# Optimization experiments

Hardware: AMD Instinct MI355X
Metric: run time of the kernel (lower is better)

The kernel has to match this reference:

```python
import jax, jax.numpy as jnp
import numpy as np

B, C, F_IN, F_OUT = 2048, 63, 250, 250
NEG_SLOPE = 0.2
N = B * C  # flattened node count


def _build_edge_index():
    # fixed fully-connected (no self) graph over the FIRST 63 nodes only
    src = np.array([i for i in range(C) for j in range(C) if i != j], dtype=np.int32)
    dst = np.array([j for i in range(C) for j in range(C) if i != j], dtype=np.int32)
    # PyG GATConv add_self_loops=True: self loop for every node (num_nodes = N)
    loops = np.arange(N, dtype=np.int32)
    src = np.concatenate([src, loops])
    dst = np.concatenate([dst, loops])
    return jnp.asarray(np.stack([src, dst]))  # [2, E]


def setup_inputs() -> dict:
    key = jax.random.key(0)
    kx, kw, ks, kd = jax.random.split(key, 4)
    x = jax.random.normal(kx, (B, 1, C, F_IN), dtype=jnp.float32)
    # GATConv params (heads=1): lin weight, att_src, att_dst, bias
    W = jax.random.normal(kw, (F_IN, F_OUT), dtype=jnp.float32) / np.sqrt(F_IN)
    att_src = jax.random.normal(ks, (F_OUT,), dtype=jnp.float32) / np.sqrt(F_OUT)
    att_dst = jax.random.normal(kd, (F_OUT,), dtype=jnp.float32) / np.sqrt(F_OUT)
    bias = jnp.zeros((F_OUT,), dtype=jnp.float32)
    return {"x": x, "W": W, "att_src": att_src, "att_dst": att_dst,
            "bias": bias, "edge_index": _build_edge_index()}


def reference(x, W, att_src, att_dst, bias, edge_index):
    b, _, c, f = x.shape
    n = b * c
    h = x.reshape(n, f) @ W                      # [N, F_OUT]
    a_src = h @ att_src                          # [N]
    a_dst = h @ att_dst                          # [N]
    src, dst = edge_index[0], edge_index[1]
    e = jax.nn.leaky_relu(a_src[src] + a_dst[dst], NEG_SLOPE)  # [E]
    # segment softmax over incoming edges of each dst node (stable)
    m = jax.ops.segment_max(e, dst, num_segments=n)
    ex = jnp.exp(e - m[dst])
    denom = jax.ops.segment_sum(ex, dst, num_segments=n)
    alpha = ex / denom[dst]                      # [E]
    out = jax.ops.segment_sum(alpha[:, None] * h[src], dst, num_segments=n)
    out = out + bias
    return out.reshape(b, 1, c, -1)              # [B,1,63,F_OUT]
```

## Files before the change

### kernel.cpp

```cpp
#include <hip/hip_runtime.h>
#include <cstdint>
#include <cstddef>

#define M_TOTAL 129024
#define KDIM    250
#define NDIM    250
#define KPAD    256
#define BM      128
#define BN      128
#define BK      64
#define LSTR    72

typedef float  f32x4  __attribute__((ext_vector_type(4)));
typedef __bf16 bf16x8 __attribute__((ext_vector_type(8)));

static __device__ __forceinline__ unsigned short f2bf(float f) {
  unsigned u = __float_as_uint(f);
  u += 0x7fffu + ((u >> 16) & 1u);
  return (unsigned short)(u >> 16);
}

static __device__ __forceinline__ float wsum(float v) {
#pragma unroll
  for (int o = 32; o > 0; o >>= 1) v += __shfl_xor(v, o, 64);
  return v;
}
static __device__ __forceinline__ float wmaxr(float v) {
#pragma unroll
  for (int o = 32; o > 0; o >>= 1) v = fmaxf(v, __shfl_xor(v, o, 64));
  return v;
}

__global__ void wcvt_kernel(const float* __restrict__ W, unsigned short* __restrict__ WT) {
  int k = threadIdx.x;
  int n = blockIdx.x;
  unsigned short v = 0;
  if (k < KDIM) v = f2bf(W[(size_t)k * NDIM + n]);
  WT[(size_t)n * KPAD + k] = v;
}

__global__ __launch_bounds__(256) void gemm_kernel(
    const float* __restrict__ X, const unsigned short* __restrict__ WT,
    const float* __restrict__ bias, float* __restrict__ out,
    float* __restrict__ h63) {
  __shared__ unsigned short lA[BM * LSTR];
  __shared__ unsigned short lB[BN * LSTR];

  const int g      = blockIdx.x;
  const int xcd    = g & 7;
  const int j      = g >> 3;
  const int m_tile = (j >> 1) * 8 + xcd;
  const int n_tile = j & 1;
  const int mBase  = m_tile * BM;
  const int nBase  = n_tile * BN;

  const int tid  = threadIdx.x;
  const int lane = tid & 63;
  const int wid  = tid >> 6;
  const int wm   = wid >> 1;
  const int wn   = wid & 1;
  const int r16  = lane & 15;
  const int quad = lane >> 4;

  f32x4 acc[4][4];
#pragma unroll
  for (int mt = 0; mt < 4; ++mt)
#pragma unroll
    for (int nt = 0; nt < 4; ++nt)
      acc[mt][nt] = f32x4{0.f, 0.f, 0.f, 0.f};

  const int aq  = tid & 15;
  const int ar0 = tid >> 4;
  const int bc  = tid & 7;
  const int br0 = tid >> 3;

  for (int kt = 0; kt < KPAD / BK; ++kt) {
    const int k0 = kt * BK;
    {
      const int gk = k0 + aq * 4;
      const bool full = (gk + 3 < KDIM);
#pragma unroll
      for (int jj = 0; jj < 8; ++jj) {
        const int row = ar0 + jj * 16;
        const float* src = X + (size_t)(mBase + row) * KDIM + gk;
        float a0, a1, a2, a3;
        if (full) {
          float2 p0 = *reinterpret_cast<const float2*>(src);
          float2 p1 = *reinterpret_cast<const float2*>(src + 2);
          a0 = p0.x; a1 = p0.y; a2 = p1.x; a3 = p1.y;
        } else {
          a0 = (gk + 0 < KDIM) ? src[0] : 0.f;
          a1 = (gk + 1 < KDIM) ? src[1] : 0.f;
          a2 = (gk + 2 < KDIM) ? src[2] : 0.f;
          a3 = (gk + 3 < KDIM) ? src[3] : 0.f;
        }
        unsigned lo = (unsigned)f2bf(a0) | ((unsigned)f2bf(a1) << 16);
        unsigned hi = (unsigned)f2bf(a2) | ((unsigned)f2bf(a3) << 16);
        *reinterpret_cast<uint2*>(&lA[row * LSTR + aq * 4]) = make_uint2(lo, hi);
      }
    }
    {
#pragma unroll
      for (int jj = 0; jj < 4; ++jj) {
        const int row = br0 + jj * 32;
        const int n = nBase + row;
        uint4 v;
        if (n < NDIM) v = *reinterpret_cast<const uint4*>(WT + (size_t)n * KPAD + k0 + bc * 8);
        else          v = make_uint4(0u, 0u, 0u, 0u);
        *reinterpret_cast<uint4*>(&lB[row * LSTR + bc * 8]) = v;
      }
    }
    __syncthreads();
#pragma unroll
    for (int ks = 0; ks < 2; ++ks) {
      const int koff = ks * 32 + quad * 8;
      bf16x8 aF[4], bF[4];
#pragma unroll
      for (int mt = 0; mt < 4; ++mt)
        aF[mt] = *reinterpret_cast<const bf16x8*>(&lA[(wm * 64 + mt * 16 + r16) * LSTR + koff]);
#pragma unroll
      for (int nt = 0; nt < 4; ++nt)
        bF[nt] = *reinterpret_cast<const bf16x8*>(&lB[(wn * 64 + nt * 16 + r16) * LSTR + koff]);
#pragma unroll
      for (int mt = 0; mt < 4; ++mt)
#pragma unroll
        for (int nt = 0; nt < 4; ++nt)
          acc[mt][nt] = __builtin_amdgcn_mfma_f32_16x16x32_bf16(aF[mt], bF[nt], acc[mt][nt], 0, 0, 0);
    }
    __syncthreads();
  }

#pragma unroll
  for (int mt = 0; mt < 4; ++mt) {
#pragma unroll
    for (int nt = 0; nt < 4; ++nt) {
      const int col = nBase + wn * 64 + nt * 16 + r16;
      if (col < NDIM) {
        const float bv = bias[col];
        const int rbase = mBase + wm * 64 + mt * 16 + quad * 4;
        f32x4 a = acc[mt][nt];
#pragma unroll
        for (int i = 0; i < 4; ++i) {
          const int r = rbase + i;
          out[(size_t)r * NDIM + col] = a[i] + bv;
          if (r < 63) h63[r * NDIM + col] = a[i];
        }
      }
    }
  }
}

__global__ void att_kernel(const float* __restrict__ h, const float* __restrict__ att_src,
                           const float* __restrict__ att_dst, const float* __restrict__ bias,
                           float* __restrict__ out) {
  const int d = blockIdx.x;
  const int tid = threadIdx.x;
  const int lane = tid & 63;
  const int wid = tid >> 6;

  __shared__ float s_asrc[64];
  __shared__ float s_adst;
  __shared__ float s_alpha[64];

  for (int s = wid; s < 63; s += 4) {
    float sum = 0.f;
    for (int f = lane; f < NDIM; f += 64) sum += h[s * NDIM + f] * att_src[f];
    sum = wsum(sum);
    if (lane == 0) s_asrc[s] = sum;
  }
  if (wid == 0) {
    float sum = 0.f;
    for (int f = lane; f < NDIM; f += 64) sum += h[d * NDIM + f] * att_dst[f];
    sum = wsum(sum);
    if (lane == 0) s_adst = sum;
  }
  __syncthreads();

  if (wid == 0) {
    float e = -__builtin_inff();
    if (lane < 63) {
      float x = s_asrc[lane] + s_adst;
      e = (x > 0.f) ? x : 0.2f * x;
    }
    const float m = wmaxr(e);
    const float p = (lane < 63) ? expf(e - m) : 0.f;
    const float den = wsum(p);
    s_alpha[lane] = p / den;
  }
  __syncthreads();

  const int f = tid;
  if (f < NDIM) {
    float o = bias[f];
    for (int s = 0; s < 63; ++s) o += s_alpha[s] * h[s * NDIM + f];
    out[(size_t)d * NDIM + f] = o;
  }
}

extern "C" void kernel_launch(void* const* d_in, const int* in_sizes, int n_in,
                              void* d_out, int out_size, void* d_ws, size_t ws_size,
                              hipStream_t stream) {
  const float* X       = (const float*)d_in[0];
  const float* W       = (const float*)d_in[1];
  const float* att_src = (const float*)d_in[2];
  const float* att_dst = (const float*)d_in[3];
  const float* bias    = (const float*)d_in[4];
  float* out = (float*)d_out;

  unsigned short* WT = (unsigned short*)d_ws;
  float* h63 = (float*)((char*)d_ws + 131072);

  wcvt_kernel<<<NDIM, KPAD, 0, stream>>>(W, WT);
  gemm_kernel<<<(M_TOTAL / BM) * 2, 256, 0, stream>>>(X, WT, bias, out, h63);
  att_kernel<<<63, 256, 0, stream>>>(h63, att_src, att_dst, bias, out);
}
```

Before: 327.4 us.

## Restructure GEMM: full-N per block, register-resident pre-swizzled W fragments

The weight conversion kernel now writes W in MFMA fragment order, so each wave loads its B fragments straight into registers (4 n-tiles × 8 k-steps). Each block now covers a 64-row M tile across the full 256-column N, which removes the duplicate reads of X from two n-tile blocks. The whole A tile is loaded at once through coalesced float2 loads, converted to bf16 and stored in LDS with a single barrier, so the K loop no longer needs LDS round trips for B. The cost is high register pressure from 32 B fragments plus 32 float2 values under launch_bounds(256,2), and less latency hiding with only one load phase.

```diff
diff --git a/kernel.cpp b/kernel.cpp
--- a/kernel.cpp
+++ b/kernel.cpp
@@ -5,11 +5,8 @@
 #define M_TOTAL 129024
 #define KDIM    250
 #define NDIM    250
-#define KPAD    256
-#define BM      128
-#define BN      128
-#define BK      64
-#define LSTR    72
+#define BM      64
+#define LASTR   264
 
 typedef float  f32x4  __attribute__((ext_vector_type(4)));
 typedef __bf16 bf16x8 __attribute__((ext_vector_type(8)));
@@ -31,37 +28,72 @@
   return v;
 }
 
-__global__ void wcvt_kernel(const float* __restrict__ W, unsigned short* __restrict__ WT) {
-  int k = threadIdx.x;
-  int n = blockIdx.x;
-  unsigned short v = 0;
-  if (k < KDIM) v = f2bf(W[(size_t)k * NDIM + n]);
-  WT[(size_t)n * KPAD + k] = v;
-}
-
-__global__ __launch_bounds__(256) void gemm_kernel(
-    const float* __restrict__ X, const unsigned short* __restrict__ WT,
+__global__ void wcvt_kernel(const float* __restrict__ W, unsigned short* __restrict__ WTf) {
+  const int f     = blockIdx.x * 256 + threadIdx.x;
+  const int lane  = f & 63;
+  const int kk    = (f >> 6) & 7;
+  const int ntile = f >> 9;
+  const int n     = ntile * 16 + (lane & 15);
+  const int k0    = kk * 32 + (lane >> 4) * 8;
+  unsigned u[4];
+#pragma unroll
+  for (int p = 0; p < 4; ++p) {
+    const int ka = k0 + 2 * p, kb = k0 + 2 * p + 1;
+    unsigned short a = (n < NDIM && ka < KDIM) ? f2bf(W[(size_t)ka * NDIM + n]) : 0;
+    unsigned short b = (n < NDIM && kb < KDIM) ? f2bf(W[(size_t)kb * NDIM + n]) : 0;
+    u[p] = (unsigned)a | ((unsigned)b << 16);
+  }
+  *reinterpret_cast<uint4*>(WTf + (size_t)f * 8) = make_uint4(u[0], u[1], u[2], u[3]);
+}
+
+__global__ __launch_bounds__(256, 2) void gemm_kernel(
+    const float* __restrict__ X, const unsigned short* __restrict__ WTf,
     const float* __restrict__ bias, float* __restrict__ out,
     float* __restrict__ h63) {
-  __shared__ unsigned short lA[BM * LSTR];
-  __shared__ unsigned short lB[BN * LSTR];
-
-  const int g      = blockIdx.x;
-  const int xcd    = g & 7;
-  const int j      = g >> 3;
-  const int m_tile = (j >> 1) * 8 + xcd;
-  const int n_tile = j & 1;
-  const int mBase  = m_tile * BM;
-  const int nBase  = n_tile * BN;
-
+  __shared__ unsigned short lA[BM * LASTR];
+
+  const int mBase = blockIdx.x * BM;
   const int tid  = threadIdx.x;
   const int lane = tid & 63;
-  const int wid  = tid >> 6;
-  const int wm   = wid >> 1;
-  const int wn   = wid & 1;
+  const int w    = tid >> 6;
   const int r16  = lane & 15;
   const int quad = lane >> 4;
 
+  const float* Xs = X + (size_t)mBase * KDIM;
+
+  float2 av[32];
+#pragma unroll
+  for (int j = 0; j < 32; ++j) {
+    const int idx = j * 256 + tid;
+    if (j < 31 || tid < 64)
+      av[j] = *reinterpret_cast<const float2*>(Xs + (size_t)idx * 2);
+  }
+
+  bf16x8 bfrag[4][8];
+#pragma unroll
+  for (int nt = 0; nt < 4; ++nt)
+#pragma unroll
+    for (int kk = 0; kk < 8; ++kk)
+      bfrag[nt][kk] = *reinterpret_cast<const bf16x8*>(
+          WTf + (size_t)((((w * 4 + nt) * 8) + kk) * 64 + lane) * 8);
+
+#pragma unroll
+  for (int j = 0; j < 32; ++j) {
+    const int idx = j * 256 + tid;
+    if (j < 31 || tid < 64) {
+      const int r = idx / 125;
+      const int c = idx - r * 125;
+      const unsigned p = (unsigned)f2bf(av[j].x) | ((unsigned)f2bf(av[j].y) << 16);
+      *reinterpret_cast<unsigned*>(&lA[r * LASTR + c * 2]) = p;
+    }
+  }
+  if (tid < 64) {
+#pragma unroll
+    for (int c = 250; c < 264; c += 2)
+      *reinterpret_cast<unsigned*>(&lA[tid * LASTR + c]) = 0u;
+  }
+  __syncthreads();
+
   f32x4 acc[4][4];
 #pragma unroll
   for (int mt = 0; mt < 4; ++mt)
@@ -69,81 +101,48 @@
     for (int nt = 0; nt < 4; ++nt)
       acc[mt][nt] = f32x4{0.f, 0.f, 0.f, 0.f};
 
-  const int aq  = tid & 15;
-  const int ar0 = tid >> 4;
-  const int bc  = tid & 7;
-  const int br0 = tid >> 3;
-
-  for (int kt = 0; kt < KPAD / BK; ++kt) {
-    const int k0 = kt * BK;
-    {
-      const int gk = k0 + aq * 4;
-      const bool full = (gk + 3 < KDIM);
-#pragma unroll
-      for (int jj = 0; jj < 8; ++jj) {
-        const int row = ar0 + jj * 16;
-        const float* src = X + (size_t)(mBase + row) * KDIM + gk;
-        float a0, a1, a2, a3;
-        if (full) {
-          float2 p0 = *reinterpret_cast<const float2*>(src);
-          float2 p1 = *reinterpret_cast<const float2*>(src + 2);
-          a0 = p0.x; a1 = p0.y; a2 = p1.x; a3 = p1.y;
-        } else {
-          a0 = (gk + 0 < KDIM) ? src[0] : 0.f;
-          a1 = (gk + 1 < KDIM) ? src[1] : 0.f;
-          a2 = (gk + 2 < KDIM) ? src[2] : 0.f;
-          a3 = (gk + 3 < KDIM) ? src[3] : 0.f;
-        }
-        unsigned lo = (unsigned)f2bf(a0) | ((unsigned)f2bf(a1) << 16);
-        unsigned hi = (unsigned)f2bf(a2) | ((unsigned)f2bf(a3) << 16);
-        *reinterpret_cast<uint2*>(&lA[row * LSTR + aq * 4]) = make_uint2(lo, hi);
+#pragma unroll
+  for (int kk = 0; kk < 8; ++kk) {
+    bf16x8 aF[4];
+#pragma unroll
+    for (int mt = 0; mt < 4; ++mt)
+      aF[mt] = *reinterpret_cast<const bf16x8*>(
+          &lA[(mt * 16 + r16) * LASTR + kk * 32 + quad * 8]);
+#pragma unroll
+    for (int mt = 0; mt < 4; ++mt)
+#pragma unroll
+      for (int nt = 0; nt < 4; ++nt)
+        acc[mt][nt] = __builtin_amdgcn_mfma_f32_16x16x32_bf16(aF[mt], bfrag[nt][kk],
+                                                              acc[mt][nt], 0, 0, 0);
+  }
+
+#pragma unroll
+  for (int nt = 0; nt < 4; ++nt) {
+    const int col = w * 64 + nt * 16 + r16;
+    if (col < NDIM) {
+      const float bv = bias[col];
+#pragma unroll
+      for (int mt = 0; mt < 4; ++mt) {
+        const int rb = mBase + mt * 16 + quad * 4;
+        f32x4 a = acc[mt][nt];
+#pragma unroll
+        for (int i = 0; i < 4; ++i)
+          out[(size_t)(rb + i) * NDIM + col] = a[i] + bv;
       }
     }
-    {
-#pragma unroll
-      for (int jj = 0; jj < 4; ++jj) {
-        const int row = br0 + jj * 32;
-        const int n = nBase + row;
-        uint4 v;
-        if (n < NDIM) v = *reinterpret_cast<const uint4*>(WT + (size_t)n * KPAD + k0 + bc * 8);
-        else          v = make_uint4(0u, 0u, 0u, 0u);
-        *reinterpret_cast<uint4*>(&lB[row * LSTR + bc * 8]) = v;
-      }
-    }
-    __syncthreads();
-#pragma unroll
-    for (int ks = 0; ks < 2; ++ks) {
-      const int koff = ks * 32 + quad * 8;
-      bf16x8 aF[4], bF[4];
-#pragma unroll
-      for (int mt = 0; mt < 4; ++mt)
-        aF[mt] = *reinterpret_cast<const bf16x8*>(&lA[(wm * 64 + mt * 16 + r16) * LSTR + koff]);
-#pragma unroll
-      for (int nt = 0; nt < 4; ++nt)
-        bF[nt] = *reinterpret_cast<const bf16x8*>(&lB[(wn * 64 + nt * 16 + r16) * LSTR + koff]);
-#pragma unroll
-      for (int mt = 0; mt < 4; ++mt)
-#pragma unroll
-        for (int nt = 0; nt < 4; ++nt)
-          acc[mt][nt] = __builtin_amdgcn_mfma_f32_16x16x32_bf16(aF[mt], bF[nt], acc[mt][nt], 0, 0, 0);
-    }
-    __syncthreads();
-  }
-
-#pragma unroll
-  for (int mt = 0; mt < 4; ++mt) {
+  }
+  if (mBase == 0) {
 #pragma unroll
     for (int nt = 0; nt < 4; ++nt) {
-      const int col = nBase + wn * 64 + nt * 16 + r16;
+      const int col = w * 64 + nt * 16 + r16;
       if (col < NDIM) {
-        const float bv = bias[col];
-        const int rbase = mBase + wm * 64 + mt * 16 + quad * 4;
-        f32x4 a = acc[mt][nt];
-#pragma unroll
-        for (int i = 0; i < 4; ++i) {
-          const int r = rbase + i;
-          out[(size_t)r * NDIM + col] = a[i] + bv;
-          if (r < 63) h63[r * NDIM + col] = a[i];
+#pragma unroll
+        for (int mt = 0; mt < 4; ++mt) {
+          const int rb = mt * 16 + quad * 4;
+          f32x4 a = acc[mt][nt];
+#pragma unroll
+          for (int i = 0; i < 4; ++i)
+            if (rb + i < 63) h63[(rb + i) * NDIM + col] = a[i];
         }
       }
     }
@@ -207,10 +206,10 @@
   const float* bias    = (const float*)d_in[4];
   float* out = (float*)d_out;
 
-  unsigned short* WT = (unsigned short*)d_ws;
+  unsigned short* WTf = (unsigned short*)d_ws;
   float* h63 = (float*)((char*)d_ws + 131072);
 
-  wcvt_kernel<<<NDIM, KPAD, 0, stream>>>(W, WT);
-  gemm_kernel<<<(M_TOTAL / BM) * 2, 256, 0, stream>>>(X, WT, bias, out, h63);
+  wcvt_kernel<<<32, 256, 0, stream>>>(W, WTf);
+  gemm_kernel<<<M_TOTAL / BM, 256, 0, stream>>>(X, WTf, bias, out, h63);
   att_kernel<<<63, 256, 0, stream>>>(h63, att_src, att_dst, bias, out);
 }
```

Result: faster. 287.2 us (-12.3%).
